# Kernel tuning notes

Measured on AMD Instinct MI355X. Metric: run time of the kernel, lower is better.

The kernel has to match this reference:

```python
import jax, jax.numpy as jnp
import numpy as np

N, D, E, H = 100000, 128, 1600000, 256  # nodes, feat dim, edges, backbone hidden
EPS = 1e-5
NEG_SLOPE = 0.01


def setup_inputs() -> dict:
    key = jax.random.key(0)
    ks = jax.random.split(key, 16)
    s = 0.02
    return {
        "x": jax.random.normal(ks[0], (N, D), dtype=jnp.float32),
        "edges": jax.random.randint(ks[1], (2, E), 0, N, dtype=jnp.int64),
        # merge layer: Linear(2D -> D)
        "W_merge": jax.random.normal(ks[2], (2 * D, D), dtype=jnp.float32) * s,
        "b_merge": jnp.zeros((D,), dtype=jnp.float32),
        # GRUCell(D, D): weights stored torch-style (3D, D)
        "W_ih": jax.random.normal(ks[3], (3 * D, D), dtype=jnp.float32) * s,
        "W_hh": jax.random.normal(ks[4], (3 * D, D), dtype=jnp.float32) * s,
        "b_ih": jnp.zeros((3 * D,), dtype=jnp.float32),
        "b_hh": jnp.zeros((3 * D,), dtype=jnp.float32),
        # backbone: Linear(D->256), BN(256), Linear(256->D), BN(D)
        "W1": jax.random.normal(ks[5], (D, H), dtype=jnp.float32) * s,
        "b1": jnp.zeros((H,), dtype=jnp.float32),
        "g1": jnp.ones((H,), dtype=jnp.float32),
        "be1": jnp.zeros((H,), dtype=jnp.float32),
        "W2": jax.random.normal(ks[6], (H, D), dtype=jnp.float32) * s,
        "b2": jnp.zeros((D,), dtype=jnp.float32),
        "g2": jnp.ones((D,), dtype=jnp.float32),
        "be2": jnp.zeros((D,), dtype=jnp.float32),
    }


def _batchnorm(y, g, b):
    m = jnp.mean(y, axis=0)
    v = jnp.var(y, axis=0)  # biased, as torch BN uses in normalization
    return g * (y - m) * jax.lax.rsqrt(v + EPS) + b


def _leaky_relu(y):
    return jnp.where(y >= 0, y, NEG_SLOPE * y)


def reference(x, edges, W_merge, b_merge, W_ih, W_hh, b_ih, b_hh,
              W1, b1, g1, be1, W2, b2, g2, be2):
    n = x.shape[0]
    src, dst = edges[0], edges[1]
    x_nbr = x[src]                                   # (E, D) gather
    agg_sum = jax.ops.segment_sum(x_nbr, dst, num_segments=n)
    agg_max = jax.ops.segment_max(x_nbr, dst, num_segments=n)
    agg_max = jnp.where(jnp.isneginf(agg_max), jnp.zeros_like(agg_max), agg_max)
    # merge 'cat' -> Linear(2D -> D)
    merged = jnp.concatenate([agg_sum, agg_max], axis=-1) @ W_merge + b_merge
    # GRUCell update: input=merged, hidden=x
    gi = merged @ W_ih.T + b_ih                      # (N, 3D)
    gh = x @ W_hh.T + b_hh                           # (N, 3D)
    i_r, i_z, i_n = jnp.split(gi, 3, axis=-1)
    h_r, h_z, h_n = jnp.split(gh, 3, axis=-1)
    r = jax.nn.sigmoid(i_r + h_r)
    z = jax.nn.sigmoid(i_z + h_z)
    nn_ = jnp.tanh(i_n + r * h_n)
    h = (1.0 - z) * nn_ + z * x
    # backbone
    y = _batchnorm(_leaky_relu(h @ W1 + b1), g1, be1)
    y = _batchnorm(_leaky_relu(y @ W2 + b2), g2, be2)
    return y
```

## Files before the change

kernel.cpp:

```cpp
#include <hip/hip_runtime.h>
#include <math.h>

#define DD 128
#define CAPB 2048
#define MAXNB 1600

typedef __attribute__((ext_vector_type(8))) short bf16x8;
typedef __attribute__((ext_vector_type(4))) float f32x4;

__device__ __forceinline__ unsigned short f2bf(float f) {
    unsigned u = __float_as_uint(f);
    unsigned r = u + 0x7FFF + ((u >> 16) & 1);
    return (unsigned short)(r >> 16);
}
__device__ __forceinline__ float bf2f(unsigned short h) {
    return __uint_as_float(((unsigned)h) << 16);
}

__global__ void k_wsfail(float* __restrict__ out, float val, int n) {
    int i = blockIdx.x * 256 + threadIdx.x;
    if (i < n) out[i] = (i == 0) ? val : 0.0f;
}

__global__ void k_setup(const int* __restrict__ e32, int* __restrict__ flag,
                        float* __restrict__ sums, int* __restrict__ gCur, int NB,
                        const float* __restrict__ W1, const float* __restrict__ W2,
                        unsigned short* __restrict__ w1T, unsigned short* __restrict__ w2T,
                        const float* __restrict__ x, unsigned short* __restrict__ AGG,
                        int total_x) {
    const int bid = blockIdx.x;
    const int t = threadIdx.x;
    if (bid == 0) {
        if (t == 0) {
            int f = 1;
            for (int i = 1; i < 16; i += 2) f &= (e32[i] == 0);
            *flag = f;
        }
        for (int i = t; i < 768; i += 256) sums[i] = 0.0f;
    } else if (bid < 8) {
        int i = (bid - 1) * 256 + t;
        if (i < NB) gCur[i] = 0;
    } else if (bid < 136) {
        int i = (bid - 8) * 256 + t;
        int j = i >> 7, k = i & 127;
        w1T[j * 128 + k] = f2bf(W1[k * 256 + j]);
    } else if (bid < 264) {
        int i = (bid - 136) * 256 + t;
        int j = i >> 8, k = i & 255;
        w2T[j * 256 + k] = f2bf(W2[k * 128 + j]);
    } else {
        int idx = (bid - 264) * 256 + t;
        if (idx < total_x) {
            int i = idx >> 7, j = idx & 127;
            AGG[(size_t)i * 384 + 256 + j] = f2bf(x[idx]);
        }
    }
}

__global__ void k_fusew(const float* __restrict__ Wm, const float* __restrict__ Wih,
                        const float* __restrict__ Whh, const float* __restrict__ bm,
                        const float* __restrict__ b_ih, const float* __restrict__ b_hh,
                        unsigned short* __restrict__ BtG, float* __restrict__ biasG) {
    const int j = blockIdx.x;
    const int c = threadIdx.x;
    const int g = j >> 7, d = j & 127;
    const int pj = ((d >> 4) << 6) + (g << 4) + (d & 15);
    float acc = 0.0f;
    if (j < 384) {
        const float* wr = Wih + (size_t)j * 128;
        const float* wc = Wm + (size_t)c * 128;
        for (int m = 0; m < 128; m++) acc += wc[m] * wr[m];
    }
    BtG[(size_t)pj * 384 + c] = f2bf(acc);
    if (c < 128) {
        float v = 0.0f;
        if (j < 256) v = Whh[(size_t)j * 128 + c];
        else if (j >= 384) v = Whh[(size_t)(j - 128) * 128 + c];
        BtG[(size_t)pj * 384 + 256 + c] = f2bf(v);
    }
    if (c == 0) {
        float b;
        if (j < 256) b = b_ih[j] + b_hh[j];
        else if (j < 384) b = b_ih[j];
        else b = b_hh[j - 128];
        if (j < 384) {
            const float* wr = Wih + (size_t)j * 128;
            float dd = 0.0f;
            for (int m = 0; m < 128; m++) dd += bm[m] * wr[m];
            b += dd;
        }
        biasG[pj] = b;
    }
}

__global__ __launch_bounds__(256) void k_bin(const void* __restrict__ edges_raw,
                                             const int* __restrict__ flag,
                                             int* __restrict__ gCur,
                                             unsigned* __restrict__ binned,
                                             int E, int Nn, int NB) {
    __shared__ int cnt_[MAXNB];
    __shared__ int cur_[MAXNB];
    const int t = threadIdx.x;
    const int e0 = blockIdx.x * 4096;
    for (int i = t; i < NB; i += 256) cnt_[i] = 0;
    __syncthreads();
    const int is64 = *flag;
    for (int k = 0; k < 16; k++) {
        int e = e0 + k * 256 + t;
        if (e < E) {
            int d = is64 ? (int)((const long long*)edges_raw)[(size_t)E + e]
                         : ((const int*)edges_raw)[(size_t)E + e];
            d = min(max(d, 0), Nn - 1);
            atomicAdd(&cnt_[d >> 6], 1);
        }
    }
    __syncthreads();
    for (int i = t; i < NB; i += 256) {
        int c = cnt_[i];
        cur_[i] = (c > 0) ? atomicAdd(&gCur[i], c) : 0;
    }
    __syncthreads();
    for (int k = 0; k < 16; k++) {
        int e = e0 + k * 256 + t;
        if (e < E) {
            int s, d;
            if (is64) {
                s = (int)((const long long*)edges_raw)[e];
                d = (int)((const long long*)edges_raw)[(size_t)E + e];
            } else {
                s = ((const int*)edges_raw)[e];
                d = ((const int*)edges_raw)[(size_t)E + e];
            }
            s = min(max(s, 0), Nn - 1);
            d = min(max(d, 0), Nn - 1);
            int b = d >> 6;
            int p = atomicAdd(&cur_[b], 1);
            if (p < CAPB)
                binned[(size_t)b * CAPB + p] = (unsigned)s | ((unsigned)(d & 63) << 23);
        }
    }
}

__global__ __launch_bounds__(256) void k_bagg(const unsigned* __restrict__ binned,
                                              const int* __restrict__ gCur,
                                              const void* __restrict__ edges_raw,
                                              const int* __restrict__ flag,
                                              unsigned short* __restrict__ AGG,
                                              int E, int Nn) {
    __shared__ unsigned ent[CAPB];
    __shared__ unsigned lsrc[CAPB];
    __shared__ int deg_[64], off_[64], cur2_[64];
    __shared__ int sa[64], sb[64];
    const int t = threadIdx.x;
    const int wave = t >> 6;
    const int lane = t & 63;
    const int b = blockIdx.x;
    const int node0 = b << 6;
    const int nloc = min(64, Nn - node0);
    const int cnt = gCur[b];
    const int c2 = lane * 2;

    if (cnt <= CAPB) {
        for (int i = t; i < cnt; i += 256) ent[i] = binned[(size_t)b * CAPB + i];
        if (t < 64) deg_[t] = 0;
        __syncthreads();
        for (int i = t; i < cnt; i += 256) atomicAdd(&deg_[ent[i] >> 23], 1);
        __syncthreads();
        if (t < 64) sa[t] = deg_[t];
        __syncthreads();
        for (int off = 1; off < 64; off <<= 1) {
            if (t < 64) sb[t] = sa[t] + ((t >= off) ? sa[t - off] : 0);
            __syncthreads();
            if (t < 64) sa[t] = sb[t];
            __syncthreads();
        }
        if (t < 64) {
            off_[t] = sa[t] - deg_[t];
            cur2_[t] = off_[t];
        }
        __syncthreads();
        for (int i = t; i < cnt; i += 256) {
            unsigned e = ent[i];
            int dl = e >> 23;
            int p = atomicAdd(&cur2_[dl], 1);
            lsrc[p] = e & 0x7FFFFF;
        }
        __syncthreads();
        for (int ln = wave; ln < nloc; ln += 4) {
            const int o = off_[ln];
            const int d = deg_[ln];
            float sx = 0.f, sy = 0.f;
            float mx = -INFINITY, my = -INFINITY;
            int e = 0;
            for (; e + 1 < d; e += 2) {
                int s0 = lsrc[o + e];
                int s1 = lsrc[o + e + 1];
                unsigned v0 = *(const unsigned*)(AGG + (size_t)s0 * 384 + 256 + c2);
                unsigned v1 = *(const unsigned*)(AGG + (size_t)s1 * 384 + 256 + c2);
                float ax = bf2f((unsigned short)(v0 & 0xffff));
                float ay = bf2f((unsigned short)(v0 >> 16));
                float bx = bf2f((unsigned short)(v1 & 0xffff));
                float by = bf2f((unsigned short)(v1 >> 16));
                sx += ax + bx; sy += ay + by;
                mx = fmaxf(mx, fmaxf(ax, bx)); my = fmaxf(my, fmaxf(ay, by));
            }
            if (e < d) {
                int s0 = lsrc[o + e];
                unsigned v0 = *(const unsigned*)(AGG + (size_t)s0 * 384 + 256 + c2);
                float ax = bf2f((unsigned short)(v0 & 0xffff));
                float ay = bf2f((unsigned short)(v0 >> 16));
                sx += ax; sy += ay;
                mx = fmaxf(mx, ax); my = fmaxf(my, ay);
            }
            if (d == 0) { mx = 0.f; my = 0.f; }
            unsigned short* row = AGG + (size_t)(node0 + ln) * 384;
            *(unsigned*)(row + c2) = (unsigned)f2bf(sx) | ((unsigned)f2bf(sy) << 16);
            *(unsigned*)(row + 128 + c2) = (unsigned)f2bf(mx) | ((unsigned)f2bf(my) << 16);
        }
    } else {
        const int is64 = *flag;
        for (int ln = wave; ln < nloc; ln += 4) {
            const int node = node0 + ln;
            float sx = 0.f, sy = 0.f;
            float mx = -INFINITY, my = -INFINITY;
            int d = 0;
            for (int e = 0; e < E; e++) {
                int dd = is64 ? (int)((const long long*)edges_raw)[(size_t)E + e]
                              : ((const int*)edges_raw)[(size_t)E + e];
                dd = min(max(dd, 0), Nn - 1);
                if (dd == node) {
                    int s = is64 ? (int)((const long long*)edges_raw)[e]
                                 : ((const int*)edges_raw)[e];
                    s = min(max(s, 0), Nn - 1);
                    unsigned v0 = *(const unsigned*)(AGG + (size_t)s * 384 + 256 + c2);
                    float ax = bf2f((unsigned short)(v0 & 0xffff));
                    float ay = bf2f((unsigned short)(v0 >> 16));
                    sx += ax; sy += ay;
                    mx = fmaxf(mx, ax); my = fmaxf(my, ay);
                    d++;
                }
            }
            if (d == 0) { mx = 0.f; my = 0.f; }
            unsigned short* row = AGG + (size_t)node * 384;
            *(unsigned*)(row + c2) = (unsigned)f2bf(sx) | ((unsigned)f2bf(sy) << 16);
            *(unsigned*)(row + 128 + c2) = (unsigned)f2bf(mx) | ((unsigned)f2bf(my) << 16);
        }
    }
}

#define GP 40

template <int AFFINE, int LEAKY, int STATS, int GRUE>
__global__ __launch_bounds__(256) void k_mgemm(
    const unsigned short* __restrict__ A, int lda,
    const unsigned short* __restrict__ Bt,
    const float* __restrict__ bias,
    const float* __restrict__ sumA, const float* __restrict__ sqA,
    const float* __restrict__ gA, const float* __restrict__ beA,
    unsigned short* __restrict__ Cb, int ldc,
    int M, int K, float* __restrict__ sumO, float* __restrict__ sqO, float invN,
    const unsigned short* __restrict__ Xb) {
    __shared__ unsigned short ABs[2 * 128 * GP];
    __shared__ float sc1[256], sh1[256];
    __shared__ float ssum[128], ssq[128];
    unsigned short* As = ABs;
    unsigned short* Bs = ABs + 128 * GP;

    const int t = threadIdx.x;
    const int lane = t & 63;
    const int wave = t >> 6;
    const int wr = (wave >> 1) * 64;
    const int wc = (wave & 1) * 64;
    const int quad = lane >> 4;
    const int l16 = lane & 15;

    const int r0 = blockIdx.y * 128;
    const int j0 = blockIdx.x * 128;

    if (AFFINE) {
        float m = sumA[t] * invN;
        float v = sqA[t] * invN - m * m;
        if (v < 0.f) v = 0.f;
        float rs = rsqrtf(v + 1e-5f);
        float sc = gA[t] * rs;
        sc1[t] = sc;
        sh1[t] = beA[t] - m * sc;
    }
    if (STATS && t < 128) { ssum[t] = 0.f; ssq[t] = 0.f; }
    if (AFFINE || STATS) __syncthreads();

    f32x4 acc[4][4];
#pragma unroll
    for (int i = 0; i < 4; i++)
#pragma unroll
        for (int j = 0; j < 4; j++) acc[i][j] = (f32x4){0.f, 0.f, 0.f, 0.f};

    const int srow = t >> 2;
    const int sk = (t & 3) * 8;

    for (int k0 = 0; k0 < K; k0 += 32) {
        union U8 { float4 f; unsigned short u[8]; } uv;
#pragma unroll
        for (int p = 0; p < 2; p++) {
            int row = p * 64 + srow;
            int gr = r0 + row;
            float4 v = make_float4(0.f, 0.f, 0.f, 0.f);
            if (gr < M) v = *(const float4*)(A + (size_t)gr * lda + k0 + sk);
            if (AFFINE) {
                uv.f = v;
#pragma unroll
                for (int q = 0; q < 8; q++) {
                    float f = bf2f(uv.u[q]) * sc1[k0 + sk + q] + sh1[k0 + sk + q];
                    uv.u[q] = f2bf(f);
                }
                v = uv.f;
            }
            *(float4*)&As[row * GP + sk] = v;
        }
#pragma unroll
        for (int p = 0; p < 2; p++) {
            int row = p * 64 + srow;
            float4 v = *(const float4*)(Bt + (size_t)(j0 + row) * K + k0 + sk);
            *(float4*)&Bs[row * GP + sk] = v;
        }
        __syncthreads();
        bf16x8 af[4], bfr[4];
#pragma unroll
        for (int i = 0; i < 4; i++) {
            af[i] = *(bf16x8*)&As[(wr + i * 16 + l16) * GP + quad * 8];
            bfr[i] = *(bf16x8*)&Bs[(wc + i * 16 + l16) * GP + quad * 8];
        }
#pragma unroll
        for (int mt = 0; mt < 4; mt++)
#pragma unroll
            for (int nt = 0; nt < 4; nt++)
                acc[mt][nt] = __builtin_amdgcn_mfma_f32_16x16x32_bf16(
                    af[mt], bfr[nt], acc[mt][nt], 0, 0, 0);
        __syncthreads();
    }

    if (GRUE) {
        const int dimb = (j0 + wc) >> 2;
        const int dloc = (wc >> 2) + l16;
        const float bR = bias[j0 + wc + l16];
        const float bZ = bias[j0 + wc + 16 + l16];
        const float bI = bias[j0 + wc + 32 + l16];
        const float bH = bias[j0 + wc + 48 + l16];
#pragma unroll
        for (int mt = 0; mt < 4; mt++) {
#pragma unroll
            for (int reg = 0; reg < 4; reg++) {
                int rloc = wr + mt * 16 + quad * 4 + reg;
                int grow = r0 + rloc;
                float r = 1.0f / (1.0f + expf(-(acc[mt][0][reg] + bR)));
                float z = 1.0f / (1.0f + expf(-(acc[mt][1][reg] + bZ)));
                float nn = tanhf(acc[mt][2][reg] + bI + r * (acc[mt][3][reg] + bH));
                float xv = 0.f;
                if (grow < M) xv = bf2f(Xb[(size_t)grow * 384 + 256 + dimb + l16]);
                float h = (1.0f - z) * nn + z * xv;
                ABs[rloc * 40 + dloc] = f2bf(h);
            }
        }
        __syncthreads();
#pragma unroll
        for (int p = 0; p < 2; p++) {
            int id = p * 256 + t;
            int rloc = id >> 2, ck = id & 3;
            int grow = r0 + rloc;
            if (grow < M)
                *(float4*)(Cb + (size_t)grow * ldc + (j0 >> 2) + ck * 8) =
                    *(const float4*)&ABs[rloc * 40 + ck * 8];
        }
        return;
    }

#pragma unroll
    for (int half = 0; half < 2; half++) {
        if (wr == half * 64) {
#pragma unroll
            for (int nt = 0; nt < 4; nt++) {
                int colLoc = wc + nt * 16 + l16;
                float bv = bias[j0 + colLoc];
                float s = 0.f, q = 0.f;
#pragma unroll
                for (int mt = 0; mt < 4; mt++) {
#pragma unroll
                    for (int reg = 0; reg < 4; reg++) {
                        int rloc = mt * 16 + quad * 4 + reg;
                        float v = acc[mt][nt][reg] + bv;
                        if (LEAKY) v = (v >= 0.f) ? v : 0.01f * v;
                        if (STATS && (r0 + half * 64 + rloc) < M) { s += v; q += v * v; }
                        ABs[rloc * 128 + colLoc] = f2bf(v);
                    }
                }
                if (STATS) {
                    atomicAdd(&ssum[colLoc], s);
                    atomicAdd(&ssq[colLoc], q);
                }
            }
        }
        __syncthreads();
#pragma unroll
        for (int p = 0; p < 4; p++) {
            int id = p * 256 + t;
            int rloc = id >> 4;
            int ck = id & 15;
            int grow = r0 + half * 64 + rloc;
            if (grow < M)
                *(float4*)(Cb + (size_t)grow * ldc + j0 + ck * 8) =
                    *(const float4*)&ABs[rloc * 128 + ck * 8];
        }
        __syncthreads();
    }
    if (STATS && t < 128) {
        atomicAdd(&sumO[j0 + t], ssum[t]);
        atomicAdd(&sqO[j0 + t], ssq[t]);
    }
}

__global__ void k_affine2(const unsigned short* __restrict__ ypre, float* __restrict__ out,
                          const float* __restrict__ sum2, const float* __restrict__ sq2,
                          const float* __restrict__ g2, const float* __restrict__ be2,
                          int total, float invN) {
    __shared__ float sc[128], sh[128];
    int t = threadIdx.x;
    if (t < 128) {
        float m = sum2[t] * invN;
        float v = sq2[t] * invN - m * m;
        if (v < 0.f) v = 0.f;
        float rs = rsqrtf(v + 1e-5f);
        float s = g2[t] * rs;
        sc[t] = s;
        sh[t] = be2[t] - m * s;
    }
    __syncthreads();
    int idx = blockIdx.x * 256 + t;
    if (idx >= total) return;
    int c = idx & 127;
    out[idx] = bf2f(ypre[idx]) * sc[c] + sh[c];
}

extern "C" void kernel_launch(void* const* d_in, const int* in_sizes, int n_in,
                              void* d_out, int out_size, void* d_ws, size_t ws_size,
                              hipStream_t stream) {
    const float* x       = (const float*)d_in[0];
    const void*  edges   = d_in[1];
    const float* W_merge = (const float*)d_in[2];
    const float* b_merge = (const float*)d_in[3];
    const float* W_ih    = (const float*)d_in[4];
    const float* W_hh    = (const float*)d_in[5];
    const float* b_ih    = (const float*)d_in[6];
    const float* b_hh    = (const float*)d_in[7];
    const float* W1      = (const float*)d_in[8];
    const float* b1      = (const float*)d_in[9];
    const float* g1      = (const float*)d_in[10];
    const float* be1     = (const float*)d_in[11];
    const float* W2      = (const float*)d_in[12];
    const float* b2      = (const float*)d_in[13];
    const float* g2      = (const float*)d_in[14];
    const float* be2     = (const float*)d_in[15];

    const int N = in_sizes[0] / DD;
    const int E = in_sizes[1] / 2;
    float* out = (float*)d_out;

    size_t need = ((size_t)640 * N + 120000) * sizeof(float);
    if (ws_size < need) {
        k_wsfail<<<(out_size + 255) / 256, 256, 0, stream>>>(
            out, (float)(ws_size >> 20), out_size);
        return;
    }

    const int NB = (N + 63) >> 6;

    float* ws = (float*)d_ws;
    unsigned short* AGG  = (unsigned short*)ws;
    unsigned short* y1b  = (unsigned short*)ws;
    unsigned short* ypre = (unsigned short*)(ws + (size_t)128 * N);
    unsigned short* hb16 = (unsigned short*)(ws + (size_t)448 * N);

    unsigned* binned = (unsigned*)(ws + (size_t)512 * N);
    int* gCur = (int*)(binned + (size_t)NB * CAPB);

    float* wbase = (float*)(gCur + NB + 64);
    unsigned short* BtG = (unsigned short*)wbase;
    unsigned short* w1T = (unsigned short*)(wbase + 98304);
    unsigned short* w2T = (unsigned short*)(wbase + 98304 + 16384);
    float* biasG = wbase + 98304 + 32768;
    float* sums  = biasG + 512;
    float* sum1 = sums, *sq1 = sums + 256, *sum2 = sums + 512, *sq2 = sums + 640;
    int*   flag  = (int*)(sums + 768);

    const int nrb  = (N + 127) / 128;
    const int ncvt = (N * DD + 255) / 256;
    const float invN = 1.0f / (float)N;

    k_setup<<<264 + ncvt, 256, 0, stream>>>(
        (const int*)edges, flag, sums, gCur, NB, W1, W2, w1T, w2T, x, AGG, N * DD);
    k_fusew<<<512, 256, 0, stream>>>(W_merge, W_ih, W_hh, b_merge, b_ih, b_hh, BtG, biasG);
    k_bin<<<(E + 4095) / 4096, 256, 0, stream>>>(edges, flag, gCur, binned, E, N, NB);
    k_bagg<<<NB, 256, 0, stream>>>(binned, gCur, edges, flag, AGG, E, N);
    k_mgemm<0, 0, 0, 1><<<dim3(4, nrb), 256, 0, stream>>>(
        AGG, 384, BtG, biasG, nullptr, nullptr, nullptr, nullptr,
        hb16, 128, N, 384, nullptr, nullptr, invN, AGG);
    k_mgemm<0, 1, 1, 0><<<dim3(2, nrb), 256, 0, stream>>>(
        hb16, 128, w1T, b1, nullptr, nullptr, nullptr, nullptr,
        y1b, 256, N, 128, sum1, sq1, invN, nullptr);
    k_mgemm<1, 1, 1, 0><<<dim3(1, nrb), 256, 0, stream>>>(
        y1b, 256, w2T, b2, sum1, sq1, g1, be1,
        ypre, 128, N, 256, sum2, sq2, invN, nullptr);
    k_affine2<<<ncvt, 256, 0, stream>>>(ypre, out, sum2, sq2, g2, be2, N * DD, invN);
}
```

Baseline: 530.1 us.

## Double-buffer GEMM tiles via direct global-to-LDS loads with XOR swizzle and XCD remap

Restructures the shared bf16 MFMA GEMM main loop to double-buffer A/B tiles in LDS, issuing the next k-slice with global_load_lds (or a register prefetch for the BN-affine path) while computing the current one. This removes one barrier per iteration and hides load latency. The padded LDS layout is replaced by an XOR-swizzled 32-wide layout to avoid bank conflicts, and workgroups are remapped so neighbouring tiles land on the same XCD for L2 reuse. LDS use rises and the out-of-range A rows are clamped rather than zeroed, which relies on those rows being discarded later.

Result: faster. 498.7 us (-5.9%).

```diff
diff --git a/kernel.cpp b/kernel.cpp
--- a/kernel.cpp
+++ b/kernel.cpp
@@ -15,6 +15,12 @@
 }
 __device__ __forceinline__ float bf2f(unsigned short h) {
     return __uint_as_float(((unsigned)h) << 16);
+}
+
+__device__ __forceinline__ void gld16(const unsigned short* g, unsigned short* l) {
+    __builtin_amdgcn_global_load_lds(
+        (const __attribute__((address_space(1))) void*)g,
+        (__attribute__((address_space(3))) void*)l, 16, 0, 0);
 }
 
 __global__ void k_wsfail(float* __restrict__ out, float val, int n) {
@@ -248,8 +254,6 @@
     }
 }
 
-#define GP 40
-
 template <int AFFINE, int LEAKY, int STATS, int GRUE>
 __global__ __launch_bounds__(256) void k_mgemm(
     const unsigned short* __restrict__ A, int lda,
@@ -260,11 +264,10 @@
     unsigned short* __restrict__ Cb, int ldc,
     int M, int K, float* __restrict__ sumO, float* __restrict__ sqO, float invN,
     const unsigned short* __restrict__ Xb) {
-    __shared__ unsigned short ABs[2 * 128 * GP];
+    __shared__ unsigned short ABs[2][2][4096];
     __shared__ float sc1[256], sh1[256];
     __shared__ float ssum[128], ssq[128];
-    unsigned short* As = ABs;
-    unsigned short* Bs = ABs + 128 * GP;
+    unsigned short* RP = &ABs[0][0][0];
 
     const int t = threadIdx.x;
     const int lane = t & 63;
@@ -273,9 +276,18 @@
     const int wc = (wave & 1) * 64;
     const int quad = lane >> 4;
     const int l16 = lane & 15;
-
-    const int r0 = blockIdx.y * 128;
-    const int j0 = blockIdx.x * 128;
+    const int sig = (l16 >> 1) & 3;
+
+    const int ncb = gridDim.x;
+    const int nwg = ncb * gridDim.y;
+    {
+    }
+    int lin = blockIdx.y * ncb + blockIdx.x;
+    const int qq = nwg >> 3, rr = nwg & 7;
+    const int xcd = lin & 7, pos = lin >> 3;
+    const int nl = (xcd < rr ? xcd * (qq + 1) : rr * (qq + 1) + (xcd - rr) * qq) + pos;
+    const int j0 = (nl % ncb) * 128;
+    const int r0 = (nl / ncb) * 128;
 
     if (AFFINE) {
         float m = sumA[t] * invN;
@@ -295,40 +307,71 @@
 #pragma unroll
         for (int j = 0; j < 4; j++) acc[i][j] = (f32x4){0.f, 0.f, 0.f, 0.f};
 
+    const int rowl = lane >> 2;
+    const int gsw8 = (((lane & 3) ^ ((lane >> 3) & 3))) * 8;
+
     const int srow = t >> 2;
-    const int sk = (t & 3) * 8;
-
+    const int sg8 = (t & 3) * 8;
+    const int swz8 = (((t & 3) ^ ((t >> 3) & 3))) * 8;
+    float4 areg[2];
+
+    auto stageA = [&](int buf, int k0) {
+#pragma unroll
+        for (int p = 0; p < 2; p++) {
+            int row = (wave * 2 + p) * 16 + rowl;
+            int gr = r0 + row;
+            if (gr >= M) gr = M - 1;
+            gld16(A + (size_t)gr * lda + k0 + gsw8,
+                  &ABs[buf][0][(wave * 2 + p) * 512]);
+        }
+    };
+    auto stageB = [&](int buf, int k0) {
+#pragma unroll
+        for (int p = 0; p < 2; p++) {
+            int row = (wave * 2 + p) * 16 + rowl;
+            gld16(Bt + (size_t)(j0 + row) * K + k0 + gsw8,
+                  &ABs[buf][1][(wave * 2 + p) * 512]);
+        }
+    };
+    auto loadA = [&](int k0) {
+#pragma unroll
+        for (int p = 0; p < 2; p++) {
+            int gr = r0 + p * 64 + srow;
+            areg[p] = make_float4(0.f, 0.f, 0.f, 0.f);
+            if (gr < M) areg[p] = *(const float4*)(A + (size_t)gr * lda + k0 + sg8);
+        }
+    };
+    auto writeA = [&](int buf, int k0) {
+        union U8 { float4 f; unsigned short u[8]; } uv;
+#pragma unroll
+        for (int p = 0; p < 2; p++) {
+            uv.f = areg[p];
+#pragma unroll
+            for (int q = 0; q < 8; q++) {
+                float f = bf2f(uv.u[q]) * sc1[k0 + sg8 + q] + sh1[k0 + sg8 + q];
+                uv.u[q] = f2bf(f);
+            }
+            *(float4*)&ABs[buf][0][(p * 64 + srow) * 32 + swz8] = uv.f;
+        }
+    };
+
+    if (AFFINE) { loadA(0); writeA(0, 0); } else stageA(0, 0);
+    stageB(0, 0);
+    __syncthreads();
+
+    int buf = 0;
     for (int k0 = 0; k0 < K; k0 += 32) {
-        union U8 { float4 f; unsigned short u[8]; } uv;
-#pragma unroll
-        for (int p = 0; p < 2; p++) {
-            int row = p * 64 + srow;
-            int gr = r0 + row;
-            float4 v = make_float4(0.f, 0.f, 0.f, 0.f);
-            if (gr < M) v = *(const float4*)(A + (size_t)gr * lda + k0 + sk);
-            if (AFFINE) {
-                uv.f = v;
-#pragma unroll
-                for (int q = 0; q < 8; q++) {
-                    float f = bf2f(uv.u[q]) * sc1[k0 + sk + q] + sh1[k0 + sk + q];
-                    uv.u[q] = f2bf(f);
-                }
-                v = uv.f;
-            }
-            *(float4*)&As[row * GP + sk] = v;
-        }
-#pragma unroll
-        for (int p = 0; p < 2; p++) {
-            int row = p * 64 + srow;
-            float4 v = *(const float4*)(Bt + (size_t)(j0 + row) * K + k0 + sk);
-            *(float4*)&Bs[row * GP + sk] = v;
-        }
-        __syncthreads();
+        const int kn = k0 + 32;
+        const bool hasNext = kn < K;
+        if (hasNext) {
+            if (AFFINE) loadA(kn); else stageA(buf ^ 1, kn);
+            stageB(buf ^ 1, kn);
+        }
         bf16x8 af[4], bfr[4];
 #pragma unroll
         for (int i = 0; i < 4; i++) {
-            af[i] = *(bf16x8*)&As[(wr + i * 16 + l16) * GP + quad * 8];
-            bfr[i] = *(bf16x8*)&Bs[(wc + i * 16 + l16) * GP + quad * 8];
+            af[i]  = *(bf16x8*)&ABs[buf][0][(wr + i * 16 + l16) * 32 + (quad ^ sig) * 8];
+            bfr[i] = *(bf16x8*)&ABs[buf][1][(wc + i * 16 + l16) * 32 + (quad ^ sig) * 8];
         }
 #pragma unroll
         for (int mt = 0; mt < 4; mt++)
@@ -336,7 +379,9 @@
             for (int nt = 0; nt < 4; nt++)
                 acc[mt][nt] = __builtin_amdgcn_mfma_f32_16x16x32_bf16(
                     af[mt], bfr[nt], acc[mt][nt], 0, 0, 0);
-        __syncthreads();
+        if (AFFINE && hasNext) writeA(buf ^ 1, kn);
+        __syncthreads();
+        buf ^= 1;
     }
 
     if (GRUE) {
@@ -358,7 +403,7 @@
                 float xv = 0.f;
                 if (grow < M) xv = bf2f(Xb[(size_t)grow * 384 + 256 + dimb + l16]);
                 float h = (1.0f - z) * nn + z * xv;
-                ABs[rloc * 40 + dloc] = f2bf(h);
+                RP[rloc * 40 + dloc] = f2bf(h);
             }
         }
         __syncthreads();
@@ -369,7 +414,7 @@
             int grow = r0 + rloc;
             if (grow < M)
                 *(float4*)(Cb + (size_t)grow * ldc + (j0 >> 2) + ck * 8) =
-                    *(const float4*)&ABs[rloc * 40 + ck * 8];
+                    *(const float4*)&RP[rloc * 40 + ck * 8];
         }
         return;
     }
@@ -390,7 +435,7 @@
                         float v = acc[mt][nt][reg] + bv;
                         if (LEAKY) v = (v >= 0.f) ? v : 0.01f * v;
                         if (STATS && (r0 + half * 64 + rloc) < M) { s += v; q += v * v; }
-                        ABs[rloc * 128 + colLoc] = f2bf(v);
+                        RP[rloc * 128 + colLoc] = f2bf(v);
                     }
                 }
                 if (STATS) {
@@ -408,7 +453,7 @@
             int grow = r0 + half * 64 + rloc;
             if (grow < M)
                 *(float4*)(Cb + (size_t)grow * ldc + j0 + ck * 8) =
-                    *(const float4*)&ABs[rloc * 128 + ck * 8];
+                    *(const float4*)&RP[rloc * 128 + ck * 8];
         }
         __syncthreads();
     }
```
